# Optimization experiments

Measured on AMD Instinct MI355X. Metric: run time of the kernel, lower is better.

## Reference

```python
import jax, jax.numpy as jnp
import numpy as np

B, S, D, H, DM, SS, A, HID = 2048, 64, 6, 4, 64, 150, 7, 256
FF = 4 * DM
DH = DM // H

def layernorm(x, g, b, eps=1e-5):
    m = jnp.mean(x, axis=-1, keepdims=True)
    v = jnp.mean((x - m) ** 2, axis=-1, keepdims=True)
    return (x - m) * jax.lax.rsqrt(v + eps) * g + b

def setup_inputs() -> dict:
    key = jax.random.key(0)
    ks = jax.random.split(key, 24)
    w = lambda k, sh: jax.random.normal(k, sh, dtype=jnp.float32) * 0.05
    inp = {
        'observation': jax.random.normal(ks[0], (B, SS), dtype=jnp.float32),
        'sequence': jax.random.normal(ks[1], (S, B, SS), dtype=jnp.float32),
        'memory': jax.random.normal(ks[2], (D, B, S, DM), dtype=jnp.float32) * 0.1,
        'length': jax.random.randint(ks[3], (1, B, 1), 0, S, dtype=jnp.int32),
        # input LayerNorm (state_size=150)
        'ln_g': jnp.ones((SS,), jnp.float32), 'ln_b': jnp.zeros((SS,), jnp.float32),
        # token_embedding replaced by Identity in source; embedding_dim(150)->dim(64) projection
        'W_emb': w(ks[4], (SS, DM)),
        # per-layer transformer params (stacked over depth)
        'ln1_g': jnp.ones((D, DM), jnp.float32), 'ln1_b': jnp.zeros((D, DM), jnp.float32),
        'ln2_g': jnp.ones((D, DM), jnp.float32), 'ln2_b': jnp.zeros((D, DM), jnp.float32),
        'Wq': w(ks[5], (D, DM, DM)), 'Wk': w(ks[6], (D, DM, DM)),
        'Wv': w(ks[7], (D, DM, DM)), 'Wo': w(ks[8], (D, DM, DM)),
        'W1': w(ks[9], (D, DM, FF)), 'b1': jnp.zeros((D, FF), jnp.float32),
        'W2': w(ks[10], (D, FF, DM)), 'b2': jnp.zeros((D, DM), jnp.float32),
        # policy MLP: dim -> 256 -> 2*action_size
        'Wp1': w(ks[11], (DM, HID)), 'bp1': jnp.zeros((HID,), jnp.float32),
        'Wp2': w(ks[12], (HID, 2 * A)), 'bp2': jnp.zeros((2 * A,), jnp.float32),
    }
    return inp

def reference(observation, sequence, memory, ln_g, ln_b, W_emb,
              ln1_g, ln1_b, ln2_g, ln2_b, Wq, Wk, Wv, Wo, W1, b1, W2, b2,
              Wp1, bp1, Wp2, bp2, length):
    # sample_forward (T == 1)
    obs = layernorm(observation, ln_g, ln_b)                      # (B,150)
    lidx = jnp.clip(length[0, :, 0], 0, S - 1)                    # (B,)
    bidx = jnp.arange(B)
    # index_put_: scatter current obs into sequence buffer at per-batch position
    seq = sequence.at[lidx, bidx].set(obs)                        # (S,B,150)
    x = jnp.einsum('bse,ed->bsd', seq.transpose(1, 0, 2), W_emb)  # (B,S,DM)
    # queries attend fully to the memory segment, causally within current segment
    causal = jnp.tril(jnp.ones((S, S), bool))
    mask = jnp.concatenate([jnp.ones((S, S), bool), causal], axis=1)  # (S, 2S)
    scale = 1.0 / np.sqrt(DH)
    new_mems = []
    for l in range(D):
        new_mems.append(x)                                        # hidden entering layer -> new memory
        h = layernorm(x, ln1_g[l], ln1_b[l])
        kv_in = jnp.concatenate([memory[l], h], axis=1)           # (B,2S,DM)
        q = (h @ Wq[l]).reshape(B, S, H, DH)
        k = (kv_in @ Wk[l]).reshape(B, 2 * S, H, DH)
        v = (kv_in @ Wv[l]).reshape(B, 2 * S, H, DH)
        scores = jnp.einsum('bqhd,bkhd->bhqk', q, k) * scale      # (B,H,S,2S)
        scores = jnp.where(mask[None, None], scores, jnp.finfo(scores.dtype).min)
        attn = jax.nn.softmax(scores, axis=-1)
        out = jnp.einsum('bhqk,bkhd->bqhd', attn, v).reshape(B, S, DM)
        x = x + out @ Wo[l]
        h2 = layernorm(x, ln2_g[l], ln2_b[l])
        x = x + jax.nn.relu(h2 @ W1[l] + b1[l]) @ W2[l] + b2[l]
    new_memory = jnp.stack(new_mems)                              # (D,B,S,DM)
    out_sb = x.transpose(1, 0, 2)                                 # (S,B,DM)
    output = out_sb[lidx, bidx]                                   # gather by length -> (B,DM)
    new_length = jnp.mod(length + 1, S)                           # (1,B,1)
    reset = (new_length[0, :, 0] == 0).astype(memory.dtype)[None, :, None, None]
    mem_out = reset * new_memory + (1.0 - reset) * memory         # masked memory reset/blend
    # policy head
    pol = jax.nn.relu(output @ Wp1 + bp1) @ Wp2 + bp2             # (B, 2A)
    std = jax.nn.softplus(pol[:, :A])
    mu = jnp.tanh(pol[:, A:])
    return (mu, std, seq, mem_out, new_length)
```

## Files before the change

### kernel.cpp

```cpp
#include <hip/hip_runtime.h>
#include <hip/hip_bf16.h>
#include <math.h>

#define NB 2048

#define LD4(p) (*(const float4*)(p))

#define O_STD 14336
#define O_SEQ 28672
#define O_MEM 19689472
#define O_LEN 70021120

#define WQT 0
#define WKT 24576
#define WVT 49152
#define WOT 73728
#define W1T 98304
#define W2T 196608
#define WET 294912

typedef __attribute__((ext_vector_type(8))) short short8v;
typedef __attribute__((ext_vector_type(4))) float f32x4;

#define MFMA(a, b, c) __builtin_amdgcn_mfma_f32_16x16x32_bf16((a), (b), (c), 0, 0, 0)

#define QSC 0.36067376022224087f

#define R_SKV   0
#define R_A1    8192
#define R_VT    12288
#define R_WO    20480
#define R_H2    24576
#define R_W2B0  28672
#define R_W2B1  32768

__device__ __forceinline__ short f2bf(float f) {
    return __builtin_bit_cast(short, (__bf16)f);
}
__device__ __forceinline__ unsigned pk2(float lo, float hi) {
    union { __hip_bfloat162 h; unsigned u; } t;
    t.h = __float22bfloat162_rn(make_float2(lo, hi));
    return t.u;
}

__global__ __launch_bounds__(256) void prep_weights(
        const float* __restrict__ Wq, const float* __restrict__ Wk,
        const float* __restrict__ Wv, const float* __restrict__ Wo,
        const float* __restrict__ W1, const float* __restrict__ W2,
        const float* __restrict__ Wemb, short* __restrict__ wsb) {
    int idx = blockIdx.x * 256 + threadIdx.x;
    {
        int l = idx >> 14, r = idx & 16383;
        { int n = r >> 6, k = r & 63;
          wsb[W1T + idx] = f2bf(W1[l * 16384 + k * 256 + n]); }
        { int n = r >> 8, k = r & 255;
          wsb[W2T + idx] = f2bf(W2[l * 16384 + k * 64 + n]); }
    }
    if (idx < 24576) {
        int l = idx >> 12, r = idx & 4095;
        int n = r >> 6, k = r & 63;
        int s = l * 4096 + k * 64 + n;
        wsb[WQT + idx] = f2bf(Wq[s]);
        wsb[WKT + idx] = f2bf(Wk[s]);
        wsb[WVT + idx] = f2bf(Wv[s]);
        wsb[WOT + idx] = f2bf(Wo[s]);
    }
    if (idx < 10240) {
        int n = idx / 160, k = idx - n * 160;
        wsb[WET + idx] = (k < 150) ? f2bf(Wemb[k * 64 + n]) : (short)0;
    }
}

__global__ __launch_bounds__(256) void copy4_kernel(const float4* __restrict__ src,
                                                    float4* __restrict__ dst, int n) {
    int i = blockIdx.x * 256 + threadIdx.x;
    if (i < n) dst[i] = src[i];
}

__global__ __launch_bounds__(256) void obs_ln_kernel(const float* __restrict__ obs,
        const float* __restrict__ g, const float* __restrict__ be,
        const int* __restrict__ len, float* __restrict__ outSeq, float* __restrict__ outLen) {
    int w = threadIdx.x >> 6, lane = threadIdx.x & 63;
    int b = blockIdx.x * 4 + w;
    const float* row = obs + (size_t)b * 150;
    float v0 = row[lane], v1 = row[64 + lane];
    float v2 = (lane < 22) ? row[128 + lane] : 0.f;
    float s = v0 + v1 + v2;
    #pragma unroll
    for (int m = 1; m <= 32; m <<= 1) s += __shfl_xor(s, m);
    float mean = s * (1.0f / 150.0f);
    float d0 = v0 - mean, d1 = v1 - mean;
    float d2 = (lane < 22) ? (v2 - mean) : 0.f;
    float q = d0 * d0 + d1 * d1 + d2 * d2;
    #pragma unroll
    for (int m = 1; m <= 32; m <<= 1) q += __shfl_xor(q, m);
    float rs = rsqrtf(q * (1.0f / 150.0f) + 1e-5f);
    int lenraw = len[b];
    int lidx = min(max(lenraw, 0), 63);
    float* orow = outSeq + ((size_t)lidx * NB + b) * 150;
    orow[lane]      = d0 * rs * g[lane] + be[lane];
    orow[64 + lane] = d1 * rs * g[64 + lane] + be[64 + lane];
    if (lane < 22) orow[128 + lane] = d2 * rs * g[128 + lane] + be[128 + lane];
    if (lane == 0) outLen[b] = (float)((lenraw + 1) & 63);
}

__global__ __launch_bounds__(256, 2) void mega_kernel(
        const float* __restrict__ seq, const float* __restrict__ memory,
        const int* __restrict__ len,
        const float* __restrict__ ln1g, const float* __restrict__ ln1b,
        const float* __restrict__ ln2g, const float* __restrict__ ln2b,
        const float* __restrict__ b1, const float* __restrict__ b2,
        const short* __restrict__ wsb,
        float* __restrict__ memOut, float* __restrict__ xrow) {
    __shared__ short L[36864];
    __shared__ float fls[576];
    float* lnp = fls;
    float* b1f = fls + 256;
    float* b2f = fls + 512;

    const int tid = threadIdx.x;
    const int b = blockIdx.x;
    const int w = tid >> 6;
    const int lane = tid & 63;
    const int g = lane >> 4;
    const int r16 = lane & 15;

    const int lenraw = len[b];
    const int lidx = min(max(lenraw, 0), 63);
    const bool reset = (((lenraw + 1) & 63) == 0);

    const int cxa = (r16 & 7) << 3;
    const int fc0 = (8 * g) ^ cxa;
    const int fc1 = (32 + 8 * g) ^ cxa;
    const int cxw = (g & 1) << 5;
    const int cxm = ((tid >> 2) & 7) << 3;

    const short8v zs = {0, 0, 0, 0, 0, 0, 0, 0};
    const f32x4 zf = {0.f, 0.f, 0.f, 0.f};

    #pragma unroll 1
    for (int j = 0; j < 16; ++j) {
        int r = w * 16 + j;
        int rb = r * 160;
        const float* srow = seq + ((size_t)r * NB + b) * 150;
        L[rb + lane]      = f2bf(srow[lane]);
        L[rb + 64 + lane] = f2bf(srow[64 + lane]);
        if (lane < 22)      L[rb + 128 + lane] = f2bf(srow[128 + lane]);
        else if (lane < 32) L[rb + 128 + lane] = 0;
    }
    {
        const int4* s4p = (const int4*)(wsb + WET);
        int4* d4p = (int4*)(L + 10240);
        #pragma unroll
        for (int i = 0; i < 5; ++i) d4p[tid + i * 256] = s4p[tid + i * 256];
    }
    __syncthreads();

    f32x4 x[4] = {zf, zf, zf, zf};
    #pragma unroll
    for (int kk = 0; kk < 5; ++kk) {
        short8v a = *(const short8v*)&L[(16 * w + r16) * 160 + kk * 32 + 8 * g];
        #pragma unroll
        for (int ct = 0; ct < 4; ++ct) {
            short8v bb = *(const short8v*)&L[10240 + (16 * ct + r16) * 160 + kk * 32 + 8 * g];
            x[ct] = MFMA(a, bb, x[ct]);
        }
    }
    __syncthreads();

    #pragma unroll 1
    for (int l = 0; l < 6; ++l) {
        auto stage_sq = [&](const short* src, int dstbase) {
            const int4* s = (const int4*)src;
            int4* d = (int4*)(L + dstbase);
            #pragma unroll
            for (int i = 0; i < 2; ++i) {
                int idx = tid + i * 256;
                d[idx ^ ((idx >> 3) & 7)] = s[idx];
            }
        };
        auto stage_w2 = [&](int kb, int dstbase) {
            int4* d = (int4*)(L + dstbase);
            #pragma unroll
            for (int i = 0; i < 2; ++i) {
                int idx = tid + i * 256;
                int sx = idx ^ ((idx >> 3) & 7);
                int n = idx >> 3, c = idx & 7;
                d[sx] = *(const int4*)&wsb[W2T + l * 16384 + n * 256 + kb * 64 + c * 8];
            }
        };

        if (tid < 64) {
            lnp[tid]       = ln1g[l * 64 + tid];
            lnp[64 + tid]  = ln1b[l * 64 + tid];
            lnp[128 + tid] = ln2g[l * 64 + tid];
            lnp[192 + tid] = ln2b[l * 64 + tid];
            b2f[tid]       = b2[l * 64 + tid];
        }
        b1f[tid] = b1[l * 256 + tid];
        {
            const float* gmem = memory + ((size_t)l * NB + b) * 4096;
            float* gout = memOut + ((size_t)l * NB + b) * 4096;
            int rr = tid >> 2, c0 = (tid & 3) * 16;
            #pragma unroll
            for (int k4 = 0; k4 < 4; ++k4) {
                float4 v = LD4(&gmem[rr * 64 + c0 + k4 * 4]);
                if (!reset) *(float4*)&gout[rr * 64 + c0 + k4 * 4] = v;
                uint2 su;
                su.x = pk2(v.x, v.y); su.y = pk2(v.z, v.w);
                *(uint2*)&L[rr * 64 + ((c0 + k4 * 4) ^ cxm)] = su;
            }
            if (reset) {
                #pragma unroll
                for (int ct = 0; ct < 4; ++ct)
                    #pragma unroll
                    for (int j = 0; j < 4; ++j)
                        gout[(16 * w + 4 * g + j) * 64 + 16 * ct + r16] = x[ct][j];
            }
        }
        stage_sq(wsb + WQT + l * 4096, R_A1);
        stage_sq(wsb + WKT + l * 4096, R_VT);
        stage_sq(wsb + WVT + l * 4096, R_VT + 4096);
        stage_sq(wsb + WOT + l * 4096, R_WO);
        stage_w2(0, R_W2B0);
        stage_w2(1, R_W2B1);
        __syncthreads();

        #pragma unroll
        for (int j = 0; j < 4; ++j) {
            float s = x[0][j] + x[1][j] + x[2][j] + x[3][j];
            s += __shfl_xor(s, 1); s += __shfl_xor(s, 2);
            s += __shfl_xor(s, 4); s += __shfl_xor(s, 8);
            float m = s * 0.015625f;
            float q = 0.f;
            #pragma unroll
            for (int ct = 0; ct < 4; ++ct) { float d = x[ct][j] - m; q += d * d; }
            q += __shfl_xor(q, 1); q += __shfl_xor(q, 2);
            q += __shfl_xor(q, 4); q += __shfl_xor(q, 8);
            float rs = rsqrtf(q * 0.015625f + 1e-5f);
            #pragma unroll
            for (int ct = 0; ct < 4; ++ct) {
                int col = 16 * ct + r16;
                float hv = (x[ct][j] - m) * rs * lnp[col] + lnp[64 + col];
                L[(64 + 16 * w + 4 * g + j) * 64 + (col ^ (cxw | (j << 3)))] = f2bf(hv);
            }
        }
        __syncthreads();

        f32x4 qa[4] = {zf, zf, zf, zf};
        f32x4 ka[2][4] = {{zf, zf, zf, zf}, {zf, zf, zf, zf}};
        #pragma unroll
        for (int kk = 0; kk < 2; ++kk) {
            const int fc = kk ? fc1 : fc0;
            short8v ah = *(const short8v*)&L[(64 + 16 * w + r16) * 64 + fc];
            short8v a0 = *(const short8v*)&L[(16 * w + r16) * 64 + fc];
            #pragma unroll
            for (int ct = 0; ct < 4; ++ct) {
                short8v bq = *(const short8v*)&L[R_A1 + (16 * ct + r16) * 64 + fc];
                short8v bk = *(const short8v*)&L[R_VT + (16 * ct + r16) * 64 + fc];
                qa[ct]    = MFMA(ah, bq, qa[ct]);
                ka[0][ct] = MFMA(a0, bk, ka[0][ct]);
                ka[1][ct] = MFMA(ah, bk, ka[1][ct]);
            }
        }
        __syncthreads();

        #pragma unroll
        for (int ct = 0; ct < 4; ++ct)
            #pragma unroll
            for (int j = 0; j < 4; ++j)
                L[R_A1 + (16 * w + 4 * g + j) * 64 + ((16 * ct + r16) ^ (cxw | (j << 3)))] =
                    f2bf(qa[ct][j] * QSC);

        f32x4 va[2][4] = {{zf, zf, zf, zf}, {zf, zf, zf, zf}};
        #pragma unroll
        for (int kk = 0; kk < 2; ++kk) {
            const int fc = kk ? fc1 : fc0;
            short8v ah = *(const short8v*)&L[(64 + 16 * w + r16) * 64 + fc];
            short8v a0 = *(const short8v*)&L[(16 * w + r16) * 64 + fc];
            #pragma unroll
            for (int ct = 0; ct < 4; ++ct) {
                short8v bv = *(const short8v*)&L[R_VT + 4096 + (16 * ct + r16) * 64 + fc];
                va[0][ct] = MFMA(a0, bv, va[0][ct]);
                va[1][ct] = MFMA(ah, bv, va[1][ct]);
            }
        }
        __syncthreads();

        #pragma unroll
        for (int ct = 0; ct < 4; ++ct) {
            #pragma unroll
            for (int j = 0; j < 4; ++j) {
                int key0 = 16 * w + 4 * g + j;
                int colw = (16 * ct + r16) ^ (cxw | (j << 3));
                L[key0 * 64 + colw] = f2bf(ka[0][ct][j]);
                L[(64 + key0) * 64 + colw] = f2bf(ka[1][ct][j]);
            }
        }
        {
            const int p0 = ((w >> 1) << 5) | (g << 3) | ((w & 1) << 2);
            const int p1 = p0 | 64;
            #pragma unroll
            for (int ct = 0; ct < 4; ++ct) {
                int rowb = R_VT + (16 * ct + r16) * 128;
                uint2 v0, v1;
                v0.x = pk2(va[0][ct][0], va[0][ct][1]);
                v0.y = pk2(va[0][ct][2], va[0][ct][3]);
                v1.x = pk2(va[1][ct][0], va[1][ct][1]);
                v1.y = pk2(va[1][ct][2], va[1][ct][3]);
                *(uint2*)&L[rowb + (p0 ^ cxa)] = v0;
                *(uint2*)&L[rowb + (p1 ^ cxa)] = v1;
            }
        }
        __syncthreads();

        const int hc = 16 * w;
        const int attc = (hc + 8 * g) ^ cxa;
        const int obc  = (hc + 4 * g) ^ cxa;
        #pragma unroll
        for (int qt = 0; qt < 4; ++qt) {
            const int KT = 5 + qt;
            short8v bQ = (g < 2) ? *(const short8v*)&L[R_A1 + (16 * qt + r16) * 64 + attc] : zs;
            f32x4 s[8];
            #pragma unroll
            for (int kt = 0; kt < 8; ++kt) if (kt < KT) {
                short8v aK = *(const short8v*)&L[(16 * kt + r16) * 64 + attc];
                s[kt] = MFMA(aK, bQ, zf);
            }
            float sum = 0.f;
            #pragma unroll
            for (int kt = 0; kt < 8; ++kt) if (kt < KT) {
                #pragma unroll
                for (int j = 0; j < 4; ++j) {
                    float e = exp2f(s[kt][j]);
                    if (kt == KT - 1) e = ((4 * g + j) > r16) ? 0.f : e;
                    s[kt][j] = e; sum += e;
                }
            }
            sum += __shfl_xor(sum, 16);
            sum += __shfl_xor(sum, 32);
            float inv = 1.0f / sum;
            f32x4 of = zf;
            const int KT2 = (KT + 1) >> 1;
            #pragma unroll
            for (int kt2 = 0; kt2 < 4; ++kt2) if (kt2 < KT2) {
                short8v aV = *(const short8v*)&L[R_VT + (hc + r16) * 128 +
                                                 ((32 * kt2 + 8 * g) ^ cxa)];
                union { short8v v; unsigned u[4]; } pb;
                const int i0 = 2 * kt2, i1 = 2 * kt2 + 1;
                pb.u[0] = pk2(s[i0][0], s[i0][1]);
                pb.u[1] = pk2(s[i0][2], s[i0][3]);
                pb.u[2] = (i1 < KT) ? pk2(s[i1][0], s[i1][1]) : 0u;
                pb.u[3] = (i1 < KT) ? pk2(s[i1][2], s[i1][3]) : 0u;
                of = MFMA(aV, pb.v, of);
            }
            uint2 ov;
            ov.x = pk2(of[0] * inv, of[1] * inv);
            ov.y = pk2(of[2] * inv, of[3] * inv);
            *(uint2*)&L[R_A1 + (16 * qt + r16) * 64 + obc] = ov;
        }
        __syncthreads();

        stage_sq(wsb + W1T + l * 16384, R_SKV);
        stage_sq(wsb + W1T + l * 16384 + 4096, R_SKV + 4096);

        #pragma unroll
        for (int kk = 0; kk < 2; ++kk) {
            const int fc = kk ? fc1 : fc0;
            short8v a = *(const short8v*)&L[R_A1 + (16 * w + r16) * 64 + fc];
            #pragma unroll
            for (int ct = 0; ct < 4; ++ct) {
                short8v bb = *(const short8v*)&L[R_WO + (16 * ct + r16) * 64 + fc];
                x[ct] = MFMA(a, bb, x[ct]);
            }
        }
        #pragma unroll
        for (int j = 0; j < 4; ++j) {
            float s = x[0][j] + x[1][j] + x[2][j] + x[3][j];
            s += __shfl_xor(s, 1); s += __shfl_xor(s, 2);
            s += __shfl_xor(s, 4); s += __shfl_xor(s, 8);
            float m = s * 0.015625f;
            float q = 0.f;
            #pragma unroll
            for (int ct = 0; ct < 4; ++ct) { float d = x[ct][j] - m; q += d * d; }
            q += __shfl_xor(q, 1); q += __shfl_xor(q, 2);
            q += __shfl_xor(q, 4); q += __shfl_xor(q, 8);
            float rs = rsqrtf(q * 0.015625f + 1e-5f);
            #pragma unroll
            for (int ct = 0; ct < 4; ++ct) {
                int col = 16 * ct + r16;
                float hv = (x[ct][j] - m) * rs * lnp[128 + col] + lnp[192 + col];
                L[R_H2 + (16 * w + 4 * g + j) * 64 + (col ^ (cxw | (j << 3)))] = f2bf(hv);
            }
        }

        auto ff_step = [&](int w1b, int w2b, int kb) {
            f32x4 tacc[4] = {zf, zf, zf, zf};
            #pragma unroll
            for (int kk = 0; kk < 2; ++kk) {
                const int fc = kk ? fc1 : fc0;
                short8v a = *(const short8v*)&L[R_H2 + (16 * w + r16) * 64 + fc];
                #pragma unroll
                for (int ct = 0; ct < 4; ++ct) {
                    short8v bb = *(const short8v*)&L[w1b + (16 * ct + r16) * 64 + fc];
                    tacc[ct] = MFMA(a, bb, tacc[ct]);
                }
            }
            #pragma unroll
            for (int ct = 0; ct < 4; ++ct)
                #pragma unroll
                for (int j = 0; j < 4; ++j) {
                    float v = fmaxf(tacc[ct][j] + b1f[kb * 64 + 16 * ct + r16], 0.f);
                    L[R_A1 + (16 * w + 4 * g + j) * 64 + ((16 * ct + r16) ^ (cxw | (j << 3)))] = f2bf(v);
                }
            #pragma unroll
            for (int kk = 0; kk < 2; ++kk) {
                const int fc = kk ? fc1 : fc0;
                short8v a = *(const short8v*)&L[R_A1 + (16 * w + r16) * 64 + fc];
                #pragma unroll
                for (int ct = 0; ct < 4; ++ct) {
                    short8v bb = *(const short8v*)&L[w2b + (16 * ct + r16) * 64 + fc];
                    x[ct] = MFMA(a, bb, x[ct]);
                }
            }
        };

        __syncthreads();
        ff_step(R_SKV, R_W2B0, 0);
        __syncthreads();
        stage_sq(wsb + W1T + l * 16384 + 2 * 4096, R_SKV);
        stage_w2(2, R_W2B0);
        ff_step(R_SKV + 4096, R_W2B1, 1);
        __syncthreads();
        stage_sq(wsb + W1T + l * 16384 + 3 * 4096, R_SKV + 4096);
        stage_w2(3, R_W2B1);
        ff_step(R_SKV, R_W2B0, 2);
        __syncthreads();
        ff_step(R_SKV + 4096, R_W2B1, 3);
        #pragma unroll
        for (int ct = 0; ct < 4; ++ct)
            #pragma unroll
            for (int j = 0; j < 4; ++j) x[ct][j] += b2f[16 * ct + r16];
        __syncthreads();
    }

    if (w == (lidx >> 4) && g == ((lidx >> 2) & 3)) {
        int j = lidx & 3;
        #pragma unroll
        for (int ct = 0; ct < 4; ++ct) {
            float v = (j == 0) ? x[ct][0] : (j == 1) ? x[ct][1] : (j == 2) ? x[ct][2] : x[ct][3];
            xrow[(size_t)b * 64 + 16 * ct + r16] = v;
        }
    }
}

__device__ __forceinline__ float softplusf(float v) {
    return fmaxf(v, 0.f) + log1pf(expf(-fabsf(v)));
}

__global__ __launch_bounds__(256) void policy_kernel(const float* __restrict__ xrow,
        const float* __restrict__ Wp1, const float* __restrict__ bp1,
        const float* __restrict__ Wp2, const float* __restrict__ bp2,
        float* __restrict__ outMu, float* __restrict__ outStd) {
    __shared__ float sx[64];
    __shared__ float sh1[256];
    const int tid = threadIdx.x;
    for (int bi = 0; bi < 16; ++bi) {
        int b = blockIdx.x * 16 + bi;
        if (tid < 64) sx[tid] = xrow[(size_t)b * 64 + tid];
        __syncthreads();
        float acc = bp1[tid];
        #pragma unroll 16
        for (int k = 0; k < 64; ++k) acc = fmaf(sx[k], Wp1[k * 256 + tid], acc);
        sh1[tid] = fmaxf(acc, 0.f);
        __syncthreads();
        if (tid < 224) {
            int j = tid >> 4, gg = tid & 15;
            float a = 0.f;
            #pragma unroll
            for (int kk = 0; kk < 16; ++kk) {
                int k = gg * 16 + kk;
                a = fmaf(sh1[k], Wp2[k * 14 + j], a);
            }
            a += __shfl_xor(a, 1); a += __shfl_xor(a, 2);
            a += __shfl_xor(a, 4); a += __shfl_xor(a, 8);
            if (gg == 0) {
                float pol = a + bp2[j];
                if (j < 7) outStd[(size_t)b * 7 + j] = softplusf(pol);
                else       outMu[(size_t)b * 7 + (j - 7)] = tanhf(pol);
            }
        }
        __syncthreads();
    }
}

extern "C" void kernel_launch(void* const* d_in, const int* in_sizes, int n_in,
                              void* d_out, int out_size, void* d_ws, size_t ws_size,
                              hipStream_t stream) {
    const float* obs   = (const float*)d_in[0];
    const float* seqIn = (const float*)d_in[1];
    const float* mem   = (const float*)d_in[2];
    const int*   len   = (const int*)d_in[3];
    const float* ln_g  = (const float*)d_in[4];
    const float* ln_b  = (const float*)d_in[5];
    const float* Wemb  = (const float*)d_in[6];
    const float* ln1g  = (const float*)d_in[7];
    const float* ln1b  = (const float*)d_in[8];
    const float* ln2g  = (const float*)d_in[9];
    const float* ln2b  = (const float*)d_in[10];
    const float* Wq    = (const float*)d_in[11];
    const float* Wk    = (const float*)d_in[12];
    const float* Wv    = (const float*)d_in[13];
    const float* Wo    = (const float*)d_in[14];
    const float* W1    = (const float*)d_in[15];
    const float* b1    = (const float*)d_in[16];
    const float* W2    = (const float*)d_in[17];
    const float* b2    = (const float*)d_in[18];
    const float* Wp1   = (const float*)d_in[19];
    const float* bp1   = (const float*)d_in[20];
    const float* Wp2   = (const float*)d_in[21];
    const float* bp2   = (const float*)d_in[22];

    float* out    = (float*)d_out;
    float* outMu  = out;
    float* outStd = out + O_STD;
    float* outSeq = out + O_SEQ;
    float* outMem = out + O_MEM;
    float* outLen = out + O_LEN;
    float* xrow   = (float*)d_ws;
    short* wsb    = (short*)((char*)d_ws + 524288);

    hipLaunchKernelGGL(prep_weights, dim3(384), dim3(256), 0, stream,
                       Wq, Wk, Wv, Wo, W1, W2, Wemb, wsb);
    hipLaunchKernelGGL(copy4_kernel, dim3(19200), dim3(256), 0, stream,
                       (const float4*)seqIn, (float4*)outSeq, 4915200);
    hipLaunchKernelGGL(obs_ln_kernel, dim3(512), dim3(256), 0, stream,
                       obs, ln_g, ln_b, len, outSeq, outLen);
    hipLaunchKernelGGL(mega_kernel, dim3(2048), dim3(256), 0, stream,
                       outSeq, mem, len, ln1g, ln1b, ln2g, ln2b, b1, b2,
                       wsb, outMem, xrow);
    hipLaunchKernelGGL(policy_kernel, dim3(128), dim3(256), 0, stream,
                       xrow, Wp1, bp1, Wp2, bp2, outMu, outStd);
}
```

Before: 497.5 us.

## Split mega_kernel work across 8 waves with column-split tiles and cross-wave layernorm

Doubles the mega_kernel block from 4 to 8 waves, so each wave owns a 16-row by 32-column slice of every tile instead of a full 64-column row block. Layernorm now computes sum and sum of squares and exchanges partial sums between wave pairs through shared memory. Attention query tiles are divided between the two wave halves, and the FFN step gains an extra barrier. The aim is more wave-level parallelism per CU to hide memory latency in the memory-bound streaming. The cost is extra barriers, and the one-pass variance is less numerically robust than the two-pass version.

```diff
diff --git a/kernel.cpp b/kernel.cpp
--- a/kernel.cpp
+++ b/kernel.cpp
@@ -104,7 +104,7 @@
     if (lane == 0) outLen[b] = (float)((lenraw + 1) & 63);
 }
 
-__global__ __launch_bounds__(256, 2) void mega_kernel(
+__global__ __launch_bounds__(512, 4) void mega_kernel(
         const float* __restrict__ seq, const float* __restrict__ memory,
         const int* __restrict__ len,
         const float* __restrict__ ln1g, const float* __restrict__ ln1b,
@@ -114,6 +114,7 @@
         float* __restrict__ memOut, float* __restrict__ xrow) {
     __shared__ short L[36864];
     __shared__ float fls[576];
+    __shared__ float2 red[2][64];
     float* lnp = fls;
     float* b1f = fls + 256;
     float* b2f = fls + 512;
@@ -124,6 +125,8 @@
     const int lane = tid & 63;
     const int g = lane >> 4;
     const int r16 = lane & 15;
+    const int wq = w & 3;
+    const int wc = w >> 2;
 
     const int lenraw = len[b];
     const int lidx = min(max(lenraw, 0), 63);
@@ -133,14 +136,13 @@
     const int fc0 = (8 * g) ^ cxa;
     const int fc1 = (32 + 8 * g) ^ cxa;
     const int cxw = (g & 1) << 5;
-    const int cxm = ((tid >> 2) & 7) << 3;
 
     const short8v zs = {0, 0, 0, 0, 0, 0, 0, 0};
     const f32x4 zf = {0.f, 0.f, 0.f, 0.f};
 
     #pragma unroll 1
-    for (int j = 0; j < 16; ++j) {
-        int r = w * 16 + j;
+    for (int j = 0; j < 8; ++j) {
+        int r = w * 8 + j;
         int rb = r * 160;
         const float* srow = seq + ((size_t)r * NB + b) * 150;
         L[rb + lane]      = f2bf(srow[lane]);
@@ -152,18 +154,21 @@
         const int4* s4p = (const int4*)(wsb + WET);
         int4* d4p = (int4*)(L + 10240);
         #pragma unroll
-        for (int i = 0; i < 5; ++i) d4p[tid + i * 256] = s4p[tid + i * 256];
+        for (int i = 0; i < 3; ++i) {
+            int idx = tid + i * 512;
+            if (idx < 1280) d4p[idx] = s4p[idx];
+        }
     }
     __syncthreads();
 
-    f32x4 x[4] = {zf, zf, zf, zf};
+    f32x4 x[2] = {zf, zf};
     #pragma unroll
     for (int kk = 0; kk < 5; ++kk) {
-        short8v a = *(const short8v*)&L[(16 * w + r16) * 160 + kk * 32 + 8 * g];
-        #pragma unroll
-        for (int ct = 0; ct < 4; ++ct) {
-            short8v bb = *(const short8v*)&L[10240 + (16 * ct + r16) * 160 + kk * 32 + 8 * g];
-            x[ct] = MFMA(a, bb, x[ct]);
+        short8v a = *(const short8v*)&L[(16 * wq + r16) * 160 + kk * 32 + 8 * g];
+        #pragma unroll
+        for (int ci = 0; ci < 2; ++ci) {
+            short8v bb = *(const short8v*)&L[10240 + (16 * (2 * wc + ci) + r16) * 160 + kk * 32 + 8 * g];
+            x[ci] = MFMA(a, bb, x[ci]);
         }
     }
     __syncthreads();
@@ -173,20 +178,40 @@
         auto stage_sq = [&](const short* src, int dstbase) {
             const int4* s = (const int4*)src;
             int4* d = (int4*)(L + dstbase);
-            #pragma unroll
-            for (int i = 0; i < 2; ++i) {
-                int idx = tid + i * 256;
-                d[idx ^ ((idx >> 3) & 7)] = s[idx];
-            }
+            d[tid ^ ((tid >> 3) & 7)] = s[tid];
         };
         auto stage_w2 = [&](int kb, int dstbase) {
             int4* d = (int4*)(L + dstbase);
-            #pragma unroll
-            for (int i = 0; i < 2; ++i) {
-                int idx = tid + i * 256;
-                int sx = idx ^ ((idx >> 3) & 7);
-                int n = idx >> 3, c = idx & 7;
-                d[sx] = *(const int4*)&wsb[W2T + l * 16384 + n * 256 + kb * 64 + c * 8];
+            int n = tid >> 3, c = tid & 7;
+            d[tid ^ ((tid >> 3) & 7)] = *(const int4*)&wsb[W2T + l * 16384 + n * 256 + kb * 64 + c * 8];
+        };
+        auto layer_norm = [&](const float* gmul, const float* gadd, int dstBase) {
+            float sv[4], qv[4];
+            #pragma unroll
+            for (int j = 0; j < 4; ++j) {
+                float s = x[0][j] + x[1][j];
+                float q = x[0][j] * x[0][j] + x[1][j] * x[1][j];
+                s += __shfl_xor(s, 1); q += __shfl_xor(q, 1);
+                s += __shfl_xor(s, 2); q += __shfl_xor(q, 2);
+                s += __shfl_xor(s, 4); q += __shfl_xor(q, 4);
+                s += __shfl_xor(s, 8); q += __shfl_xor(q, 8);
+                sv[j] = s; qv[j] = q;
+                if (r16 == 0) red[wc][16 * wq + 4 * g + j] = make_float2(s, q);
+            }
+            __syncthreads();
+            #pragma unroll
+            for (int j = 0; j < 4; ++j) {
+                int R = 16 * wq + 4 * g + j;
+                float2 o = red[1 - wc][R];
+                float m = (sv[j] + o.x) * 0.015625f;
+                float var = (qv[j] + o.y) * 0.015625f - m * m;
+                float rs = rsqrtf(var + 1e-5f);
+                #pragma unroll
+                for (int ci = 0; ci < 2; ++ci) {
+                    int col = 16 * (2 * wc + ci) + r16;
+                    float hv = (x[ci][j] - m) * rs * gmul[col] + gadd[col];
+                    L[dstBase + R * 64 + (col ^ (cxw | (j << 3)))] = f2bf(hv);
+                }
             }
         };
 
@@ -197,25 +222,27 @@
             lnp[192 + tid] = ln2b[l * 64 + tid];
             b2f[tid]       = b2[l * 64 + tid];
         }
-        b1f[tid] = b1[l * 256 + tid];
+        if (tid < 256) b1f[tid] = b1[l * 256 + tid];
         {
             const float* gmem = memory + ((size_t)l * NB + b) * 4096;
             float* gout = memOut + ((size_t)l * NB + b) * 4096;
-            int rr = tid >> 2, c0 = (tid & 3) * 16;
-            #pragma unroll
-            for (int k4 = 0; k4 < 4; ++k4) {
-                float4 v = LD4(&gmem[rr * 64 + c0 + k4 * 4]);
-                if (!reset) *(float4*)&gout[rr * 64 + c0 + k4 * 4] = v;
+            int rr = tid >> 3, c0 = (tid & 7) * 8;
+            const int cxm = (rr & 7) << 3;
+            #pragma unroll
+            for (int k4 = 0; k4 < 2; ++k4) {
+                int c = c0 + k4 * 4;
+                float4 v = LD4(&gmem[rr * 64 + c]);
+                if (!reset) *(float4*)&gout[rr * 64 + c] = v;
                 uint2 su;
                 su.x = pk2(v.x, v.y); su.y = pk2(v.z, v.w);
-                *(uint2*)&L[rr * 64 + ((c0 + k4 * 4) ^ cxm)] = su;
+                *(uint2*)&L[rr * 64 + (c ^ cxm)] = su;
             }
             if (reset) {
                 #pragma unroll
-                for (int ct = 0; ct < 4; ++ct)
+                for (int ci = 0; ci < 2; ++ci)
                     #pragma unroll
                     for (int j = 0; j < 4; ++j)
-                        gout[(16 * w + 4 * g + j) * 64 + 16 * ct + r16] = x[ct][j];
+                        gout[(16 * wq + 4 * g + j) * 64 + 16 * (2 * wc + ci) + r16] = x[ci][j];
             }
         }
         stage_sq(wsb + WQT + l * 4096, R_A1);
@@ -226,138 +253,123 @@
         stage_w2(1, R_W2B1);
         __syncthreads();
 
-        #pragma unroll
-        for (int j = 0; j < 4; ++j) {
-            float s = x[0][j] + x[1][j] + x[2][j] + x[3][j];
-            s += __shfl_xor(s, 1); s += __shfl_xor(s, 2);
-            s += __shfl_xor(s, 4); s += __shfl_xor(s, 8);
-            float m = s * 0.015625f;
-            float q = 0.f;
-            #pragma unroll
-            for (int ct = 0; ct < 4; ++ct) { float d = x[ct][j] - m; q += d * d; }
-            q += __shfl_xor(q, 1); q += __shfl_xor(q, 2);
-            q += __shfl_xor(q, 4); q += __shfl_xor(q, 8);
-            float rs = rsqrtf(q * 0.015625f + 1e-5f);
-            #pragma unroll
-            for (int ct = 0; ct < 4; ++ct) {
-                int col = 16 * ct + r16;
-                float hv = (x[ct][j] - m) * rs * lnp[col] + lnp[64 + col];
-                L[(64 + 16 * w + 4 * g + j) * 64 + (col ^ (cxw | (j << 3)))] = f2bf(hv);
-            }
-        }
-        __syncthreads();
-
-        f32x4 qa[4] = {zf, zf, zf, zf};
-        f32x4 ka[2][4] = {{zf, zf, zf, zf}, {zf, zf, zf, zf}};
+        layer_norm(lnp, lnp + 64, 4096);
+        __syncthreads();
+
+        f32x4 qa[2] = {zf, zf};
+        f32x4 ka[2][2] = {{zf, zf}, {zf, zf}};
         #pragma unroll
         for (int kk = 0; kk < 2; ++kk) {
             const int fc = kk ? fc1 : fc0;
-            short8v ah = *(const short8v*)&L[(64 + 16 * w + r16) * 64 + fc];
-            short8v a0 = *(const short8v*)&L[(16 * w + r16) * 64 + fc];
-            #pragma unroll
-            for (int ct = 0; ct < 4; ++ct) {
+            short8v ah = *(const short8v*)&L[(64 + 16 * wq + r16) * 64 + fc];
+            short8v a0 = *(const short8v*)&L[(16 * wq + r16) * 64 + fc];
+            #pragma unroll
+            for (int ci = 0; ci < 2; ++ci) {
+                int ct = 2 * wc + ci;
                 short8v bq = *(const short8v*)&L[R_A1 + (16 * ct + r16) * 64 + fc];
                 short8v bk = *(const short8v*)&L[R_VT + (16 * ct + r16) * 64 + fc];
-                qa[ct]    = MFMA(ah, bq, qa[ct]);
-                ka[0][ct] = MFMA(a0, bk, ka[0][ct]);
-                ka[1][ct] = MFMA(ah, bk, ka[1][ct]);
-            }
-        }
-        __syncthreads();
-
-        #pragma unroll
-        for (int ct = 0; ct < 4; ++ct)
+                qa[ci]    = MFMA(ah, bq, qa[ci]);
+                ka[0][ci] = MFMA(a0, bk, ka[0][ci]);
+                ka[1][ci] = MFMA(ah, bk, ka[1][ci]);
+            }
+        }
+        __syncthreads();
+
+        #pragma unroll
+        for (int ci = 0; ci < 2; ++ci)
             #pragma unroll
             for (int j = 0; j < 4; ++j)
-                L[R_A1 + (16 * w + 4 * g + j) * 64 + ((16 * ct + r16) ^ (cxw | (j << 3)))] =
-                    f2bf(qa[ct][j] * QSC);
-
-        f32x4 va[2][4] = {{zf, zf, zf, zf}, {zf, zf, zf, zf}};
+                L[R_A1 + (16 * wq + 4 * g + j) * 64 +
+                  ((16 * (2 * wc + ci) + r16) ^ (cxw | (j << 3)))] = f2bf(qa[ci][j] * QSC);
+
+        f32x4 va[2][2] = {{zf, zf}, {zf, zf}};
         #pragma unroll
         for (int kk = 0; kk < 2; ++kk) {
             const int fc = kk ? fc1 : fc0;
-            short8v ah = *(const short8v*)&L[(64 + 16 * w + r16) * 64 + fc];
-            short8v a0 = *(const short8v*)&L[(16 * w + r16) * 64 + fc];
-            #pragma unroll
-            for (int ct = 0; ct < 4; ++ct) {
-                short8v bv = *(const short8v*)&L[R_VT + 4096 + (16 * ct + r16) * 64 + fc];
-                va[0][ct] = MFMA(a0, bv, va[0][ct]);
-                va[1][ct] = MFMA(ah, bv, va[1][ct]);
-            }
-        }
-        __syncthreads();
-
-        #pragma unroll
-        for (int ct = 0; ct < 4; ++ct) {
+            short8v ah = *(const short8v*)&L[(64 + 16 * wq + r16) * 64 + fc];
+            short8v a0 = *(const short8v*)&L[(16 * wq + r16) * 64 + fc];
+            #pragma unroll
+            for (int ci = 0; ci < 2; ++ci) {
+                short8v bv = *(const short8v*)&L[R_VT + 4096 + (16 * (2 * wc + ci) + r16) * 64 + fc];
+                va[0][ci] = MFMA(a0, bv, va[0][ci]);
+                va[1][ci] = MFMA(ah, bv, va[1][ci]);
+            }
+        }
+        __syncthreads();
+
+        #pragma unroll
+        for (int ci = 0; ci < 2; ++ci) {
             #pragma unroll
             for (int j = 0; j < 4; ++j) {
-                int key0 = 16 * w + 4 * g + j;
-                int colw = (16 * ct + r16) ^ (cxw | (j << 3));
-                L[key0 * 64 + colw] = f2bf(ka[0][ct][j]);
-                L[(64 + key0) * 64 + colw] = f2bf(ka[1][ct][j]);
+                int key0 = 16 * wq + 4 * g + j;
+                int colw = (16 * (2 * wc + ci) + r16) ^ (cxw | (j << 3));
+                L[key0 * 64 + colw] = f2bf(ka[0][ci][j]);
+                L[(64 + key0) * 64 + colw] = f2bf(ka[1][ci][j]);
             }
         }
         {
-            const int p0 = ((w >> 1) << 5) | (g << 3) | ((w & 1) << 2);
+            const int p0 = ((wq >> 1) << 5) | (g << 3) | ((wq & 1) << 2);
             const int p1 = p0 | 64;
             #pragma unroll
-            for (int ct = 0; ct < 4; ++ct) {
-                int rowb = R_VT + (16 * ct + r16) * 128;
+            for (int ci = 0; ci < 2; ++ci) {
+                int rowb = R_VT + (16 * (2 * wc + ci) + r16) * 128;
                 uint2 v0, v1;
-                v0.x = pk2(va[0][ct][0], va[0][ct][1]);
-                v0.y = pk2(va[0][ct][2], va[0][ct][3]);
-                v1.x = pk2(va[1][ct][0], va[1][ct][1]);
-                v1.y = pk2(va[1][ct][2], va[1][ct][3]);
+                v0.x = pk2(va[0][ci][0], va[0][ci][1]);
+                v0.y = pk2(va[0][ci][2], va[0][ci][3]);
+                v1.x = pk2(va[1][ci][0], va[1][ci][1]);
+                v1.y = pk2(va[1][ci][2], va[1][ci][3]);
                 *(uint2*)&L[rowb + (p0 ^ cxa)] = v0;
                 *(uint2*)&L[rowb + (p1 ^ cxa)] = v1;
             }
         }
         __syncthreads();
 
-        const int hc = 16 * w;
-        const int attc = (hc + 8 * g) ^ cxa;
-        const int obc  = (hc + 4 * g) ^ cxa;
-        #pragma unroll
-        for (int qt = 0; qt < 4; ++qt) {
-            const int KT = 5 + qt;
-            short8v bQ = (g < 2) ? *(const short8v*)&L[R_A1 + (16 * qt + r16) * 64 + attc] : zs;
-            f32x4 s[8];
-            #pragma unroll
-            for (int kt = 0; kt < 8; ++kt) if (kt < KT) {
-                short8v aK = *(const short8v*)&L[(16 * kt + r16) * 64 + attc];
-                s[kt] = MFMA(aK, bQ, zf);
-            }
-            float sum = 0.f;
-            #pragma unroll
-            for (int kt = 0; kt < 8; ++kt) if (kt < KT) {
-                #pragma unroll
-                for (int j = 0; j < 4; ++j) {
-                    float e = exp2f(s[kt][j]);
-                    if (kt == KT - 1) e = ((4 * g + j) > r16) ? 0.f : e;
-                    s[kt][j] = e; sum += e;
-                }
-            }
-            sum += __shfl_xor(sum, 16);
-            sum += __shfl_xor(sum, 32);
-            float inv = 1.0f / sum;
-            f32x4 of = zf;
-            const int KT2 = (KT + 1) >> 1;
-            #pragma unroll
-            for (int kt2 = 0; kt2 < 4; ++kt2) if (kt2 < KT2) {
-                short8v aV = *(const short8v*)&L[R_VT + (hc + r16) * 128 +
-                                                 ((32 * kt2 + 8 * g) ^ cxa)];
-                union { short8v v; unsigned u[4]; } pb;
-                const int i0 = 2 * kt2, i1 = 2 * kt2 + 1;
-                pb.u[0] = pk2(s[i0][0], s[i0][1]);
-                pb.u[1] = pk2(s[i0][2], s[i0][3]);
-                pb.u[2] = (i1 < KT) ? pk2(s[i1][0], s[i1][1]) : 0u;
-                pb.u[3] = (i1 < KT) ? pk2(s[i1][2], s[i1][3]) : 0u;
-                of = MFMA(aV, pb.v, of);
-            }
-            uint2 ov;
-            ov.x = pk2(of[0] * inv, of[1] * inv);
-            ov.y = pk2(of[2] * inv, of[3] * inv);
-            *(uint2*)&L[R_A1 + (16 * qt + r16) * 64 + obc] = ov;
+        {
+            const int hc = 16 * (w & 3);
+            const int attc = (hc + 8 * g) ^ cxa;
+            const int obc  = (hc + 4 * g) ^ cxa;
+            auto do_attn = [&](int qt, int KT) {
+                short8v bQ = (g < 2) ? *(const short8v*)&L[R_A1 + (16 * qt + r16) * 64 + attc] : zs;
+                f32x4 s[8];
+                #pragma unroll
+                for (int kt = 0; kt < 8; ++kt) if (kt < KT) {
+                    short8v aK = *(const short8v*)&L[(16 * kt + r16) * 64 + attc];
+                    s[kt] = MFMA(aK, bQ, zf);
+                }
+                float sum = 0.f;
+                #pragma unroll
+                for (int kt = 0; kt < 8; ++kt) if (kt < KT) {
+                    #pragma unroll
+                    for (int j = 0; j < 4; ++j) {
+                        float e = exp2f(s[kt][j]);
+                        if (kt == KT - 1) e = ((4 * g + j) > r16) ? 0.f : e;
+                        s[kt][j] = e; sum += e;
+                    }
+                }
+                sum += __shfl_xor(sum, 16);
+                sum += __shfl_xor(sum, 32);
+                float inv = 1.0f / sum;
+                f32x4 of = zf;
+                const int KT2 = (KT + 1) >> 1;
+                #pragma unroll
+                for (int kt2 = 0; kt2 < 4; ++kt2) if (kt2 < KT2) {
+                    short8v aV = *(const short8v*)&L[R_VT + (hc + r16) * 128 +
+                                                     ((32 * kt2 + 8 * g) ^ cxa)];
+                    union { short8v v; unsigned u[4]; } pb;
+                    const int i0 = 2 * kt2, i1 = 2 * kt2 + 1;
+                    pb.u[0] = pk2(s[i0][0], s[i0][1]);
+                    pb.u[1] = pk2(s[i0][2], s[i0][3]);
+                    pb.u[2] = (i1 < KT) ? pk2(s[i1][0], s[i1][1]) : 0u;
+                    pb.u[3] = (i1 < KT) ? pk2(s[i1][2], s[i1][3]) : 0u;
+                    of = MFMA(aV, pb.v, of);
+                }
+                uint2 ov;
+                ov.x = pk2(of[0] * inv, of[1] * inv);
+                ov.y = pk2(of[2] * inv, of[3] * inv);
+                *(uint2*)&L[R_A1 + (16 * qt + r16) * 64 + obc] = ov;
+            };
+            if (wc == 0) { do_attn(0, 5); do_attn(1, 6); }
+            else         { do_attn(2, 7); do_attn(3, 8); }
         }
         __syncthreads();
 
@@ -367,60 +379,44 @@
         #pragma unroll
         for (int kk = 0; kk < 2; ++kk) {
             const int fc = kk ? fc1 : fc0;
-            short8v a = *(const short8v*)&L[R_A1 + (16 * w + r16) * 64 + fc];
-            #pragma unroll
-            for (int ct = 0; ct < 4; ++ct) {
-                short8v bb = *(const short8v*)&L[R_WO + (16 * ct + r16) * 64 + fc];
-                x[ct] = MFMA(a, bb, x[ct]);
-            }
-        }
-        #pragma unroll
-        for (int j = 0; j < 4; ++j) {
-            float s = x[0][j] + x[1][j] + x[2][j] + x[3][j];
-            s += __shfl_xor(s, 1); s += __shfl_xor(s, 2);
-            s += __shfl_xor(s, 4); s += __shfl_xor(s, 8);
-            float m = s * 0.015625f;
-            float q = 0.f;
-            #pragma unroll
-            for (int ct = 0; ct < 4; ++ct) { float d = x[ct][j] - m; q += d * d; }
-            q += __shfl_xor(q, 1); q += __shfl_xor(q, 2);
-            q += __shfl_xor(q, 4); q += __shfl_xor(q, 8);
-            float rs = rsqrtf(q * 0.015625f + 1e-5f);
-            #pragma unroll
-            for (int ct = 0; ct < 4; ++ct) {
-                int col = 16 * ct + r16;
-                float hv = (x[ct][j] - m) * rs * lnp[128 + col] + lnp[192 + col];
-                L[R_H2 + (16 * w + 4 * g + j) * 64 + (col ^ (cxw | (j << 3)))] = f2bf(hv);
-            }
-        }
+            short8v a = *(const short8v*)&L[R_A1 + (16 * wq + r16) * 64 + fc];
+            #pragma unroll
+            for (int ci = 0; ci < 2; ++ci) {
+                short8v bb = *(const short8v*)&L[R_WO + (16 * (2 * wc + ci) + r16) * 64 + fc];
+                x[ci] = MFMA(a, bb, x[ci]);
+            }
+        }
+        layer_norm(lnp + 128, lnp + 192, R_H2);
 
         auto ff_step = [&](int w1b, int w2b, int kb) {
-            f32x4 tacc[4] = {zf, zf, zf, zf};
+            f32x4 tacc[2] = {zf, zf};
             #pragma unroll
             for (int kk = 0; kk < 2; ++kk) {
                 const int fc = kk ? fc1 : fc0;
-                short8v a = *(const short8v*)&L[R_H2 + (16 * w + r16) * 64 + fc];
-                #pragma unroll
-                for (int ct = 0; ct < 4; ++ct) {
-                    short8v bb = *(const short8v*)&L[w1b + (16 * ct + r16) * 64 + fc];
-                    tacc[ct] = MFMA(a, bb, tacc[ct]);
-                }
-            }
-            #pragma unroll
-            for (int ct = 0; ct < 4; ++ct)
+                short8v a = *(const short8v*)&L[R_H2 + (16 * wq + r16) * 64 + fc];
+                #pragma unroll
+                for (int ci = 0; ci < 2; ++ci) {
+                    short8v bb = *(const short8v*)&L[w1b + (16 * (2 * wc + ci) + r16) * 64 + fc];
+                    tacc[ci] = MFMA(a, bb, tacc[ci]);
+                }
+            }
+            #pragma unroll
+            for (int ci = 0; ci < 2; ++ci)
                 #pragma unroll
                 for (int j = 0; j < 4; ++j) {
-                    float v = fmaxf(tacc[ct][j] + b1f[kb * 64 + 16 * ct + r16], 0.f);
-                    L[R_A1 + (16 * w + 4 * g + j) * 64 + ((16 * ct + r16) ^ (cxw | (j << 3)))] = f2bf(v);
-                }
+                    int ct = 2 * wc + ci;
+                    float v = fmaxf(tacc[ci][j] + b1f[kb * 64 + 16 * ct + r16], 0.f);
+                    L[R_A1 + (16 * wq + 4 * g + j) * 64 + ((16 * ct + r16) ^ (cxw | (j << 3)))] = f2bf(v);
+                }
+            __syncthreads();
             #pragma unroll
             for (int kk = 0; kk < 2; ++kk) {
                 const int fc = kk ? fc1 : fc0;
-                short8v a = *(const short8v*)&L[R_A1 + (16 * w + r16) * 64 + fc];
-                #pragma unroll
-                for (int ct = 0; ct < 4; ++ct) {
-                    short8v bb = *(const short8v*)&L[w2b + (16 * ct + r16) * 64 + fc];
-                    x[ct] = MFMA(a, bb, x[ct]);
+                short8v a = *(const short8v*)&L[R_A1 + (16 * wq + r16) * 64 + fc];
+                #pragma unroll
+                for (int ci = 0; ci < 2; ++ci) {
+                    short8v bb = *(const short8v*)&L[w2b + (16 * (2 * wc + ci) + r16) * 64 + fc];
+                    x[ci] = MFMA(a, bb, x[ci]);
                 }
             }
         };
@@ -438,18 +434,18 @@
         __syncthreads();
         ff_step(R_SKV + 4096, R_W2B1, 3);
         #pragma unroll
-        for (int ct = 0; ct < 4; ++ct)
-            #pragma unroll
-            for (int j = 0; j < 4; ++j) x[ct][j] += b2f[16 * ct + r16];
-        __syncthreads();
-    }
-
-    if (w == (lidx >> 4) && g == ((lidx >> 2) & 3)) {
+        for (int ci = 0; ci < 2; ++ci)
+            #pragma unroll
+            for (int j = 0; j < 4; ++j) x[ci][j] += b2f[16 * (2 * wc + ci) + r16];
+        __syncthreads();
+    }
+
+    if (wq == (lidx >> 4) && g == ((lidx >> 2) & 3)) {
         int j = lidx & 3;
         #pragma unroll
-        for (int ct = 0; ct < 4; ++ct) {
-            float v = (j == 0) ? x[ct][0] : (j == 1) ? x[ct][1] : (j == 2) ? x[ct][2] : x[ct][3];
-            xrow[(size_t)b * 64 + 16 * ct + r16] = v;
+        for (int ci = 0; ci < 2; ++ci) {
+            float v = (j == 0) ? x[ci][0] : (j == 1) ? x[ci][1] : (j == 2) ? x[ci][2] : x[ci][3];
+            xrow[(size_t)b * 64 + 16 * (2 * wc + ci) + r16] = v;
         }
     }
 }
@@ -536,7 +532,7 @@
                        (const float4*)seqIn, (float4*)outSeq, 4915200);
     hipLaunchKernelGGL(obs_ln_kernel, dim3(512), dim3(256), 0, stream,
                        obs, ln_g, ln_b, len, outSeq, outLen);
-    hipLaunchKernelGGL(mega_kernel, dim3(2048), dim3(256), 0, stream,
+    hipLaunchKernelGGL(mega_kernel, dim3(2048), dim3(512), 0, stream,
                        outSeq, mem, len, ln1g, ln1b, ln2g, ln2b, b1, b2,
                        wsb, outMem, xrow);
     hipLaunchKernelGGL(policy_kernel, dim3(128), dim3(256), 0, stream,
```

Result: slower. 652.4 us (+31.1%).
